# Kernel optimization log

Measured on AMD Instinct MI355X. Metric: run time of the kernel, lower is better.

Reference implementation:

```python
import jax, jax.numpy as jnp
import numpy as np

N, FEATS, HIDDEN, CLASSES, E, DEPTH = 100000, 512, 64, 64, 3200000, 10


def setup_inputs() -> dict:
    key = jax.random.key(0)
    ks = jax.random.split(key, 8)
    x = jax.random.normal(ks[0], (N, FEATS), jnp.float32)
    edges = jax.random.randint(ks[1], (2, E), 0, N, jnp.int32)
    mask = jax.random.randint(ks[2], (N,), 0, 2, jnp.int32)
    labels = jax.random.randint(ks[3], (N,), 0, CLASSES, jnp.int32)
    s1 = 1.0 / np.sqrt(FEATS)
    s2 = 1.0 / np.sqrt(HIDDEN)
    w1 = jax.random.uniform(ks[4], (FEATS, HIDDEN), jnp.float32, -s1, s1)
    b1 = jax.random.uniform(ks[5], (HIDDEN,), jnp.float32, -s1, s1)
    w2 = jax.random.uniform(ks[6], (HIDDEN, CLASSES), jnp.float32, -s2, s2)
    b2 = jax.random.uniform(ks[7], (CLASSES,), jnp.float32, -s2, s2)
    return {"x": x, "w1": w1, "b1": b1, "w2": w2, "b2": b2,
            "edges": edges, "mask": mask, "labels": labels}


def _graph_conv(h, src, dst, norm):
    # out[v] = sum over edges (u -> v) of h[u] / sqrt(deg_out(u) * deg_in(v))
    return jax.ops.segment_sum(h[src] * norm[:, None], dst, num_segments=N)


def reference(x, w1, b1, w2, b2, edges, mask, labels):
    src, dst = edges[0], edges[1]
    ones = jnp.ones((E,), jnp.float32)
    deg_out = jnp.maximum(jax.ops.segment_sum(ones, src, num_segments=N), 1.0)
    deg_in = jnp.maximum(jax.ops.segment_sum(ones, dst, num_segments=N), 1.0)
    norm = jax.lax.rsqrt(deg_out[src] * deg_in[dst])  # [E]

    # eval path: dropout is identity
    h = jax.nn.relu(x @ w1 + b1)
    p = jax.nn.softmax(h @ w2 + b2, axis=1)  # [N, C]

    train = mask != 0  # [N] bool
    onehot = jax.nn.one_hot(labels, CLASSES, dtype=p.dtype) * train[:, None]
    err = onehot - p
    h0 = err
    tm = train[:, None]
    for _ in range(DEPTH):
        err = _graph_conv(err, src, dst, norm)
        err = jnp.where(tm, h0, err)  # err[nz,:] = h0[nz,:]

    out = p + err
    h0 = out
    for _ in range(DEPTH):
        out = _graph_conv(out, src, dst, norm) * 0.9 + h0 * 0.1
    return jnp.log(out + 1.0)
```

## Files before the change

kernel.cpp:

```cpp
#include <hip/hip_runtime.h>
#include <hip/hip_fp16.h>
#include <math.h>

#define NN    100000
#define FEATS 512
#define HID   64
#define EE    3200000
#define WIDTH 96

__global__ void ell_build(const int* __restrict__ src, const int* __restrict__ dst,
                          int* __restrict__ deg_out, int* __restrict__ fill,
                          int* __restrict__ col) {
  int stride = gridDim.x * blockDim.x;
  int tid = blockIdx.x * blockDim.x + threadIdx.x;
  const int4* s4 = reinterpret_cast<const int4*>(src);
  const int4* d4 = reinterpret_cast<const int4*>(dst);
  for (int q = tid; q < EE / 4; q += stride) {
    int4 s = s4[q];
    int4 d = d4[q];
    atomicAdd(&deg_out[s.x], 1);
    atomicAdd(&deg_out[s.y], 1);
    atomicAdd(&deg_out[s.z], 1);
    atomicAdd(&deg_out[s.w], 1);
    int p0 = atomicAdd(&fill[d.x], 1);
    if (p0 < WIDTH) col[(size_t)d.x * WIDTH + p0] = s.x;
    int p1 = atomicAdd(&fill[d.y], 1);
    if (p1 < WIDTH) col[(size_t)d.y * WIDTH + p1] = s.y;
    int p2 = atomicAdd(&fill[d.z], 1);
    if (p2 < WIDTH) col[(size_t)d.z * WIDTH + p2] = s.z;
    int p3 = atomicAdd(&fill[d.w], 1);
    if (p3 < WIDTH) col[(size_t)d.w * WIDTH + p3] = s.w;
  }
}

__global__ void node_prep(const int* __restrict__ dout, const int* __restrict__ din,
                          float* __restrict__ r_out, float* __restrict__ rr,
                          float* __restrict__ inv_r_out) {
  int i = blockIdx.x * 256 + threadIdx.x;
  if (i >= NN) return;
  int a = dout[i]; if (a < 1) a = 1;
  int b = din[i];  if (b < 1) b = 1;
  float ro = rsqrtf((float)a);
  r_out[i] = ro;
  rr[i] = ro * rsqrtf((float)b);
  inv_r_out[i] = sqrtf((float)a);
}

__global__ __launch_bounds__(256) void fused_mlp(const float* __restrict__ x,
                                                 const float* __restrict__ w1,
                                                 const float* __restrict__ b1,
                                                 const float* __restrict__ w2,
                                                 const float* __restrict__ b2,
                                                 const int* __restrict__ mask,
                                                 const int* __restrict__ labels,
                                                 const float* __restrict__ r_out,
                                                 float* __restrict__ p,
                                                 __half* __restrict__ err0) {
  __shared__ float hs[64 * 65];
  __shared__ float w2s[64 * 64];
  float* xs = w2s;
  float* ws = w2s + 64 * 17;
  int t = threadIdx.x;
  int row0 = blockIdx.x * 64;
  int tx = t & 15, ty = t >> 4;
  int lr = t >> 2, lq = t & 3;
  int wk = t >> 4, wc = (t & 15) * 4;
  float acc[4][4] = {};
  for (int k0 = 0; k0 < FEATS; k0 += 16) {
    float4 xv = make_float4(0.f, 0.f, 0.f, 0.f);
    int gr = row0 + lr;
    if (gr < NN) xv = *reinterpret_cast<const float4*>(x + (size_t)gr * FEATS + k0 + lq * 4);
    float4 wv = *reinterpret_cast<const float4*>(w1 + (size_t)(k0 + wk) * HID + wc);
    xs[lr * 17 + lq * 4 + 0] = xv.x; xs[lr * 17 + lq * 4 + 1] = xv.y;
    xs[lr * 17 + lq * 4 + 2] = xv.z; xs[lr * 17 + lq * 4 + 3] = xv.w;
    ws[wk * 64 + wc + 0] = wv.x; ws[wk * 64 + wc + 1] = wv.y;
    ws[wk * 64 + wc + 2] = wv.z; ws[wk * 64 + wc + 3] = wv.w;
    __syncthreads();
#pragma unroll
    for (int kk = 0; kk < 16; ++kk) {
      float a[4], b[4];
#pragma unroll
      for (int ii = 0; ii < 4; ++ii) a[ii] = xs[(ty * 4 + ii) * 17 + kk];
#pragma unroll
      for (int jj = 0; jj < 4; ++jj) b[jj] = ws[kk * 64 + tx * 4 + jj];
#pragma unroll
      for (int ii = 0; ii < 4; ++ii)
#pragma unroll
        for (int jj = 0; jj < 4; ++jj) acc[ii][jj] = fmaf(a[ii], b[jj], acc[ii][jj]);
    }
    __syncthreads();
  }
  float bb[4];
#pragma unroll
  for (int jj = 0; jj < 4; ++jj) bb[jj] = b1[tx * 4 + jj];
#pragma unroll
  for (int ii = 0; ii < 4; ++ii)
#pragma unroll
    for (int jj = 0; jj < 4; ++jj)
      hs[(ty * 4 + ii) * 65 + tx * 4 + jj] = fmaxf(acc[ii][jj] + bb[jj], 0.f);
#pragma unroll
  for (int q = 0; q < 16; ++q) w2s[t + q * 256] = w2[t + q * 256];
  __syncthreads();
  float lg[4][4];
#pragma unroll
  for (int jj = 0; jj < 4; ++jj) {
    float b2v = b2[tx * 4 + jj];
#pragma unroll
    for (int ii = 0; ii < 4; ++ii) lg[ii][jj] = b2v;
  }
#pragma unroll 4
  for (int k = 0; k < 64; ++k) {
    float hk[4];
#pragma unroll
    for (int ii = 0; ii < 4; ++ii) hk[ii] = hs[(ty * 4 + ii) * 65 + k];
#pragma unroll
    for (int jj = 0; jj < 4; ++jj) {
      float wv2 = w2s[k * 64 + tx * 4 + jj];
#pragma unroll
      for (int ii = 0; ii < 4; ++ii) lg[ii][jj] = fmaf(hk[ii], wv2, lg[ii][jj]);
    }
  }
  __syncthreads();
#pragma unroll
  for (int ii = 0; ii < 4; ++ii)
#pragma unroll
    for (int jj = 0; jj < 4; ++jj)
      hs[(ty * 4 + ii) * 65 + tx * 4 + jj] = lg[ii][jj];
  __syncthreads();
  int wv_ = t >> 6, lane = t & 63;
  for (int q = 0; q < 16; ++q) {
    int r = wv_ * 16 + q;
    int i = row0 + r;
    if (i >= NN) break;
    float v = hs[r * 65 + lane];
    float m = v;
#pragma unroll
    for (int off = 32; off >= 1; off >>= 1) m = fmaxf(m, __shfl_xor(m, off));
    float e = expf(v - m);
    float s = e;
#pragma unroll
    for (int off = 32; off >= 1; off >>= 1) s += __shfl_xor(s, off);
    float pv = e / s;
    size_t off64 = (size_t)i * 64 + lane;
    p[off64] = pv;
    float oh = (mask[i] != 0 && labels[i] == lane) ? 1.f : 0.f;
    err0[off64] = __float2half(r_out[i] * (oh - pv));
  }
}

template <int MODE>
__global__ __launch_bounds__(256) void conv_h(const int* __restrict__ fill,
                                              const int* __restrict__ col,
                                              const float* __restrict__ rr,
                                              const float* __restrict__ inv_r_out,
                                              const int* __restrict__ mask,
                                              const __half* __restrict__ in,
                                              const __half* __restrict__ uinit,
                                              __half* __restrict__ out,
                                              float* __restrict__ fout) {
  int wid = (blockIdx.x * 256 + threadIdx.x) >> 6;
  int lane = threadIdx.x & 63;
  if (wid >= NN) return;
  size_t off = (size_t)wid * 64 + lane;
  if (MODE == 1) {
    if (mask[wid] != 0) { out[off] = in[off]; return; }
  }
  int cnt = fill[wid];
  if (cnt > WIDTH) cnt = WIDTH;
  const int* cp = col + (size_t)wid * WIDTH;
  float sum = 0.f;
  for (int e = 0; e < cnt; e += 32) {
    int cc[32];
#pragma unroll
    for (int q = 0; q < 8; ++q) {
      int4 c4 = *reinterpret_cast<const int4*>(cp + e + q * 4);
      cc[q * 4 + 0] = c4.x; cc[q * 4 + 1] = c4.y;
      cc[q * 4 + 2] = c4.z; cc[q * 4 + 3] = c4.w;
    }
    int rem = cnt - e;
    int c0 = cc[0];
#pragma unroll
    for (int j = 0; j < 32; ++j)
      if (j >= rem) cc[j] = c0;
    float vv[32];
#pragma unroll
    for (int j = 0; j < 32; ++j) vv[j] = __half2float(in[(size_t)cc[j] * 64 + lane]);
#pragma unroll
    for (int j = 0; j < 32; ++j) sum += (j < rem) ? vv[j] : 0.f;
  }
  if (MODE == 1) {
    out[off] = __float2half(rr[wid] * sum);
  } else {
    float f = fmaf(0.9f * rr[wid], sum, 0.1f * __half2float(uinit[off]));
    if (MODE == 2) out[off] = __float2half(f);
    else           fout[off] = logf(f * inv_r_out[wid] + 1.f);
  }
}

__global__ void combine_kernel(const float* __restrict__ p, const __half* __restrict__ t10,
                               const float* __restrict__ r_out, __half* __restrict__ u) {
  int idx = blockIdx.x * 256 + threadIdx.x;
  if (idx >= NN * 32) return;
  int i = idx >> 5;
  float ro = r_out[i];
  float2 pv = reinterpret_cast<const float2*>(p)[idx];
  __half2 tv = reinterpret_cast<const __half2*>(t10)[idx];
  float2 tf = __half22float2(tv);
  reinterpret_cast<__half2*>(u)[idx] =
      __floats2half2_rn(fmaf(ro, pv.x, tf.x), fmaf(ro, pv.y, tf.y));
}

extern "C" void kernel_launch(void* const* d_in, const int* in_sizes, int n_in,
                              void* d_out, int out_size, void* d_ws, size_t ws_size,
                              hipStream_t stream) {
  const float* x      = (const float*)d_in[0];
  const float* w1     = (const float*)d_in[1];
  const float* b1     = (const float*)d_in[2];
  const float* w2     = (const float*)d_in[3];
  const float* b2     = (const float*)d_in[4];
  const int*   edges  = (const int*)d_in[5];
  const int*   mask   = (const int*)d_in[6];
  const int*   labels = (const int*)d_in[7];
  const int*   src = edges;
  const int*   dst = edges + EE;

  char* w = (char*)d_ws;
  auto alloc = [&](size_t bytes) -> char* {
    char* pp = w;
    w += (bytes + 255) & ~(size_t)255;
    return pp;
  };
  int*    deg_out = (int*)alloc((size_t)NN * 4);
  int*    fillc   = (int*)alloc((size_t)NN * 4);
  float*  r_out   = (float*)alloc((size_t)NN * 4);
  float*  rr      = (float*)alloc((size_t)NN * 4);
  float*  inv_ro  = (float*)alloc((size_t)NN * 4);
  float*  P       = (float*)alloc((size_t)NN * HID * 4);
  __half* E       = (__half*)alloc((size_t)NN * HID * 2);
  __half* F       = (__half*)alloc((size_t)NN * HID * 2);
  __half* U       = (__half*)alloc((size_t)NN * HID * 2);
  int*    col     = (int*)alloc((size_t)NN * WIDTH * 4);

  hipMemsetAsync(deg_out, 0, (size_t)((char*)r_out - (char*)deg_out), stream);

  const int SCAN_NB = (NN + 255) / 256;
  const int CONV_GRID = (NN + 3) / 4;

  ell_build<<<2048, 256, 0, stream>>>(src, dst, deg_out, fillc, col);
  node_prep<<<SCAN_NB, 256, 0, stream>>>(deg_out, fillc, r_out, rr, inv_ro);
  fused_mlp<<<(NN + 63) / 64, 256, 0, stream>>>(x, w1, b1, w2, b2, mask, labels,
                                                r_out, P, E);

#define CONV(MODE, IN, UI, OUT, FOUT)                                           \
  conv_h<MODE><<<CONV_GRID, 256, 0, stream>>>(fillc, col, rr, inv_ro, mask,     \
                                              IN, UI, OUT, FOUT)

  {
    __half* in = E; __half* out = F;
    for (int it = 0; it < 10; ++it) {
      CONV(1, in, (__half*)nullptr, out, (float*)nullptr);
      __half* tmp = in; in = out; out = tmp;
    }
  }

  combine_kernel<<<(NN * 32 + 255) / 256, 256, 0, stream>>>(P, E, r_out, U);

  CONV(2, U, U, F, (float*)nullptr);
  {
    __half* in = F; __half* out = E;
    for (int it = 1; it < 9; ++it) {
      CONV(2, in, U, out, (float*)nullptr);
      __half* tmp = in; in = out; out = tmp;
    }
  }
  CONV(3, F, U, (__half*)nullptr, (float*)d_out);
#undef CONV
}
```

Before: 2.014 ms.

## Bucket ELL columns by source-node slice and process slices in phases

```diff
diff --git a/kernel.cpp b/kernel.cpp
--- a/kernel.cpp
+++ b/kernel.cpp
@@ -6,10 +6,16 @@
 #define FEATS 512
 #define HID   64
 #define EE    3200000
-#define WIDTH 96
+#define NBUCK 3
+#define BUCKW 32
+#define ROWW  (NBUCK * BUCKW)
+#define SLICE 33334
+#define CONV_NB  768
+#define WPB   4
+#define NPW   33
 
 __global__ void ell_build(const int* __restrict__ src, const int* __restrict__ dst,
-                          int* __restrict__ deg_out, int* __restrict__ fill,
+                          int* __restrict__ deg_out, int* __restrict__ fill3,
                           int* __restrict__ col) {
   int stride = gridDim.x * blockDim.x;
   int tid = blockIdx.x * blockDim.x + threadIdx.x;
@@ -22,24 +28,26 @@
     atomicAdd(&deg_out[s.y], 1);
     atomicAdd(&deg_out[s.z], 1);
     atomicAdd(&deg_out[s.w], 1);
-    int p0 = atomicAdd(&fill[d.x], 1);
-    if (p0 < WIDTH) col[(size_t)d.x * WIDTH + p0] = s.x;
-    int p1 = atomicAdd(&fill[d.y], 1);
-    if (p1 < WIDTH) col[(size_t)d.y * WIDTH + p1] = s.y;
-    int p2 = atomicAdd(&fill[d.z], 1);
-    if (p2 < WIDTH) col[(size_t)d.z * WIDTH + p2] = s.z;
-    int p3 = atomicAdd(&fill[d.w], 1);
-    if (p3 < WIDTH) col[(size_t)d.w * WIDTH + p3] = s.w;
-  }
-}
-
-__global__ void node_prep(const int* __restrict__ dout, const int* __restrict__ din,
+    int b0 = s.x / SLICE, b1 = s.y / SLICE, b2 = s.z / SLICE, b3 = s.w / SLICE;
+    int p0 = atomicAdd(&fill3[d.x * NBUCK + b0], 1);
+    if (p0 < BUCKW) col[(size_t)d.x * ROWW + b0 * BUCKW + p0] = s.x;
+    int p1 = atomicAdd(&fill3[d.y * NBUCK + b1], 1);
+    if (p1 < BUCKW) col[(size_t)d.y * ROWW + b1 * BUCKW + p1] = s.y;
+    int p2 = atomicAdd(&fill3[d.z * NBUCK + b2], 1);
+    if (p2 < BUCKW) col[(size_t)d.z * ROWW + b2 * BUCKW + p2] = s.z;
+    int p3 = atomicAdd(&fill3[d.w * NBUCK + b3], 1);
+    if (p3 < BUCKW) col[(size_t)d.w * ROWW + b3 * BUCKW + p3] = s.w;
+  }
+}
+
+__global__ void node_prep(const int* __restrict__ dout, const int* __restrict__ fill3,
                           float* __restrict__ r_out, float* __restrict__ rr,
                           float* __restrict__ inv_r_out) {
   int i = blockIdx.x * 256 + threadIdx.x;
   if (i >= NN) return;
   int a = dout[i]; if (a < 1) a = 1;
-  int b = din[i];  if (b < 1) b = 1;
+  int b = fill3[i * NBUCK] + fill3[i * NBUCK + 1] + fill3[i * NBUCK + 2];
+  if (b < 1) b = 1;
   float ro = rsqrtf((float)a);
   r_out[i] = ro;
   rr[i] = ro * rsqrtf((float)b);
@@ -149,7 +157,7 @@
 }
 
 template <int MODE>
-__global__ __launch_bounds__(256) void conv_h(const int* __restrict__ fill,
+__global__ __launch_bounds__(256) void conv_p(const int* __restrict__ fill3,
                                               const int* __restrict__ col,
                                               const float* __restrict__ rr,
                                               const float* __restrict__ inv_r_out,
@@ -158,42 +166,57 @@
                                               const __half* __restrict__ uinit,
                                               __half* __restrict__ out,
                                               float* __restrict__ fout) {
-  int wid = (blockIdx.x * 256 + threadIdx.x) >> 6;
-  int lane = threadIdx.x & 63;
-  if (wid >= NN) return;
-  size_t off = (size_t)wid * 64 + lane;
-  if (MODE == 1) {
-    if (mask[wid] != 0) { out[off] = in[off]; return; }
-  }
-  int cnt = fill[wid];
-  if (cnt > WIDTH) cnt = WIDTH;
-  const int* cp = col + (size_t)wid * WIDTH;
-  float sum = 0.f;
-  for (int e = 0; e < cnt; e += 32) {
-    int cc[32];
-#pragma unroll
-    for (int q = 0; q < 8; ++q) {
-      int4 c4 = *reinterpret_cast<const int4*>(cp + e + q * 4);
-      cc[q * 4 + 0] = c4.x; cc[q * 4 + 1] = c4.y;
-      cc[q * 4 + 2] = c4.z; cc[q * 4 + 3] = c4.w;
-    }
-    int rem = cnt - e;
-    int c0 = cc[0];
-#pragma unroll
-    for (int j = 0; j < 32; ++j)
-      if (j >= rem) cc[j] = c0;
-    float vv[32];
-#pragma unroll
-    for (int j = 0; j < 32; ++j) vv[j] = __half2float(in[(size_t)cc[j] * 64 + lane]);
-#pragma unroll
-    for (int j = 0; j < 32; ++j) sum += (j < rem) ? vv[j] : 0.f;
-  }
-  if (MODE == 1) {
-    out[off] = __float2half(rr[wid] * sum);
-  } else {
-    float f = fmaf(0.9f * rr[wid], sum, 0.1f * __half2float(uinit[off]));
-    if (MODE == 2) out[off] = __float2half(f);
-    else           fout[off] = logf(f * inv_r_out[wid] + 1.f);
+  __shared__ float sacc[WPB * NPW * 64];
+  int t = threadIdx.x;
+  int w = t >> 6, lane = t & 63;
+  int gw = blockIdx.x * WPB + w;
+  int n0 = gw * NPW;
+  float* sbase = sacc + (w * NPW) * 64;
+  for (int j = 0; j < NPW; ++j) sbase[j * 64 + lane] = 0.f;
+  for (int p = 0; p < NBUCK; ++p) {
+    for (int j = 0; j < NPW; ++j) {
+      int node = n0 + j;
+      if (node >= NN) break;
+      if (MODE == 1 && mask[node] != 0) continue;
+      int cnt = fill3[node * NBUCK + p];
+      if (cnt > BUCKW) cnt = BUCKW;
+      if (cnt == 0) continue;
+      const int* cp = col + (size_t)node * ROWW + p * BUCKW;
+      float rsum = 0.f;
+      for (int e = 0; e < cnt; e += 16) {
+        int cc[16];
+#pragma unroll
+        for (int q = 0; q < 4; ++q) {
+          int4 c4 = *reinterpret_cast<const int4*>(cp + e + q * 4);
+          cc[q * 4 + 0] = c4.x; cc[q * 4 + 1] = c4.y;
+          cc[q * 4 + 2] = c4.z; cc[q * 4 + 3] = c4.w;
+        }
+        int rem = cnt - e;
+        int c0 = cc[0];
+#pragma unroll
+        for (int jj = 0; jj < 16; ++jj)
+          if (jj >= rem) cc[jj] = c0;
+        float vv[16];
+#pragma unroll
+        for (int jj = 0; jj < 16; ++jj) vv[jj] = __half2float(in[(size_t)cc[jj] * 64 + lane]);
+#pragma unroll
+        for (int jj = 0; jj < 16; ++jj) rsum += (jj < rem) ? vv[jj] : 0.f;
+      }
+      sbase[j * 64 + lane] += rsum;
+    }
+  }
+  for (int j = 0; j < NPW; ++j) {
+    int node = n0 + j;
+    if (node >= NN) break;
+    size_t off = (size_t)node * 64 + lane;
+    float sum = sbase[j * 64 + lane];
+    if (MODE == 1) {
+      out[off] = (mask[node] != 0) ? in[off] : __float2half(rr[node] * sum);
+    } else {
+      float f = fmaf(0.9f * rr[node], sum, 0.1f * __half2float(uinit[off]));
+      if (MODE == 2) out[off] = __float2half(f);
+      else           fout[off] = logf(f * inv_r_out[node] + 1.f);
+    }
   }
 }
 
@@ -231,7 +254,7 @@
     return pp;
   };
   int*    deg_out = (int*)alloc((size_t)NN * 4);
-  int*    fillc   = (int*)alloc((size_t)NN * 4);
+  int*    fill3   = (int*)alloc((size_t)NN * NBUCK * 4);
   float*  r_out   = (float*)alloc((size_t)NN * 4);
   float*  rr      = (float*)alloc((size_t)NN * 4);
   float*  inv_ro  = (float*)alloc((size_t)NN * 4);
@@ -239,21 +262,20 @@
   __half* E       = (__half*)alloc((size_t)NN * HID * 2);
   __half* F       = (__half*)alloc((size_t)NN * HID * 2);
   __half* U       = (__half*)alloc((size_t)NN * HID * 2);
-  int*    col     = (int*)alloc((size_t)NN * WIDTH * 4);
+  int*    col     = (int*)alloc((size_t)NN * ROWW * 4 + 256);
 
   hipMemsetAsync(deg_out, 0, (size_t)((char*)r_out - (char*)deg_out), stream);
 
   const int SCAN_NB = (NN + 255) / 256;
-  const int CONV_GRID = (NN + 3) / 4;
-
-  ell_build<<<2048, 256, 0, stream>>>(src, dst, deg_out, fillc, col);
-  node_prep<<<SCAN_NB, 256, 0, stream>>>(deg_out, fillc, r_out, rr, inv_ro);
+
+  ell_build<<<2048, 256, 0, stream>>>(src, dst, deg_out, fill3, col);
+  node_prep<<<SCAN_NB, 256, 0, stream>>>(deg_out, fill3, r_out, rr, inv_ro);
   fused_mlp<<<(NN + 63) / 64, 256, 0, stream>>>(x, w1, b1, w2, b2, mask, labels,
                                                 r_out, P, E);
 
-#define CONV(MODE, IN, UI, OUT, FOUT)                                           \
-  conv_h<MODE><<<CONV_GRID, 256, 0, stream>>>(fillc, col, rr, inv_ro, mask,     \
-                                              IN, UI, OUT, FOUT)
+#define CONV(MODE, IN, UI, OUT, FOUT)                                        \
+  conv_p<MODE><<<CONV_NB, 256, 0, stream>>>(fill3, col, rr, inv_ro, mask,    \
+                                            IN, UI, OUT, FOUT)
 
   {
     __half* in = E; __half* out = F;
```

Result: slower. 3.606 ms (+79.1%).
